# Kernel tuning notes

Measured on AMD Instinct MI355X. Metric: run time of the kernel, lower is better.

The kernel has to match this reference:

```python
import jax, jax.numpy as jnp
import numpy as np

B, S, H = 2, 2048, 1024
NH = 16
HD = H // NH  # 64
EPS = 1e-6
NEG = -1e9


def setup_inputs() -> dict:
    key = jax.random.key(0)
    ks = jax.random.split(key, 6)
    scale = 1.0 / np.sqrt(H)
    return {
        "enc": jax.random.normal(ks[0], (B, S, H), dtype=jnp.float32),
        "mask": jnp.ones((B, 1, S, S), dtype=jnp.float32),
        "W_Q": jax.random.normal(ks[1], (H, H), dtype=jnp.float32) * scale,
        "W_K": jax.random.normal(ks[2], (H, H), dtype=jnp.float32) * scale,
        "W_V": jax.random.normal(ks[3], (H, H), dtype=jnp.float32) * scale,
        "W_O": jax.random.normal(ks[4], (H, H), dtype=jnp.float32) * scale,
        "ln_w": jnp.ones((H,), dtype=jnp.float32),
        "ln_b": jnp.zeros((H,), dtype=jnp.float32),
    }


def reference(enc, mask, W_Q, W_K, W_V, W_O, ln_w, ln_b):
    residual = enc
    # projections (nn.Linear: x @ W.T), split heads -> [B, NH, S, HD]
    def proj(W):
        return (enc @ W.T).reshape(B, S, NH, HD).transpose(0, 2, 1, 3)
    Q, K, V = proj(W_Q), proj(W_K), proj(W_V)
    # scaled dot-product attention with mask
    attn_score = jnp.einsum("bhqd,bhkd->bhqk", Q, K) / jnp.sqrt(jnp.float32(HD))
    attn_score = jnp.where(mask == 0, jnp.float32(NEG), attn_score)
    attn_dist = jax.nn.softmax(attn_score, axis=-1)  # dropout_prob=0 -> identity
    out = jnp.einsum("bhqk,bhkd->bhqd", attn_dist, V)
    out = out.transpose(0, 2, 1, 3).reshape(B, S, H)
    # output projection + residual + LayerNorm(eps=1e-6)
    x = out @ W_O.T + residual
    mu = jnp.mean(x, axis=-1, keepdims=True)
    var = jnp.var(x, axis=-1, keepdims=True)
    y = (x - mu) / jnp.sqrt(var + EPS) * ln_w + ln_b
    return (y, attn_dist)
```

## Files before the change

### kernel.cpp

```cpp
#include <hip/hip_runtime.h>
#include <hip/hip_bf16.h>
#include <cstdint>

#define B_   2
#define S_   2048
#define H_   1024
#define NH_  16
#define HD_  64
#define YSIZE (B_*S_*H_)
#define ATTN_PER_BH ((size_t)S_*S_)

typedef __bf16 bf16x8 __attribute__((ext_vector_type(8)));
typedef __bf16 bf16x4_t __attribute__((ext_vector_type(4)));
typedef float f32x4 __attribute__((ext_vector_type(4)));

#define MFMA(a, b, c) __builtin_amdgcn_mfma_f32_16x16x32_bf16((a), (b), (c), 0, 0, 0)

__device__ __forceinline__ void gl2lds16(const void* g, void* lds) {
    __builtin_amdgcn_global_load_lds(
        (__attribute__((address_space(1))) void*)g,
        (__attribute__((address_space(3))) void*)lds,
        16, 0, 0);
}

__global__ __launch_bounds__(256) void k_convert(
    const float* __restrict__ enc, const float* __restrict__ wq,
    const float* __restrict__ wk, const float* __restrict__ wv,
    const float* __restrict__ wo,
    __bf16* __restrict__ encb, __bf16* __restrict__ wqb,
    __bf16* __restrict__ wkb, __bf16* __restrict__ wvb,
    __bf16* __restrict__ wob)
{
    size_t i = ((size_t)blockIdx.x * 256 + threadIdx.x) * 4;
    const float* src; __bf16* dst; size_t off;
    if (i < (size_t)YSIZE) { src = enc; dst = encb; off = i; }
    else {
        size_t j = i - YSIZE; int w = (int)(j >> 20); off = j & 1048575u;
        if      (w == 0) { src = wq; dst = wqb; }
        else if (w == 1) { src = wk; dst = wkb; }
        else if (w == 2) { src = wv; dst = wvb; }
        else             { src = wo; dst = wob; }
    }
    float4 v = *(const float4*)(src + off);
    bf16x4_t o;
    o[0] = (__bf16)v.x; o[1] = (__bf16)v.y; o[2] = (__bf16)v.z; o[3] = (__bf16)v.w;
    *(bf16x4_t*)(dst + off) = o;
}

template<int OUTF32>
__global__ __launch_bounds__(256) void k_gemm_nt(
    const __bf16* __restrict__ A, const __bf16* __restrict__ Bm,
    void* __restrict__ Cout, const float* __restrict__ resid,
    int K, int Nrs,
    unsigned Md, unsigned s1, unsigned s2, unsigned Nd, unsigned s3, unsigned s4)
{
    __shared__ __bf16 As[128 * 32];
    __shared__ __bf16 Bs[128 * 32];
    const int tid = threadIdx.x, l = tid & 63, w = tid >> 6;
    const int quad = l >> 4, l16 = l & 15;
    const int row0 = blockIdx.y * 128, col0 = blockIdx.x * 128;
    const int mbase = (w >> 1) * 64, nbase = (w & 1) * 64;

    f32x4 acc[4][4] = {};

    for (int k0 = 0; k0 < K; k0 += 32) {
#pragma unroll
        for (int i = 0; i < 2; ++i) {
            int lc = (w * 2 + i) * 64 + l;
            int r = lc >> 2, p = lc & 3;
            int c = p ^ ((r >> 1) & 3);
            gl2lds16(A + ((size_t)(row0 + r) * K + k0 + c * 8), As + (w * 2 + i) * 512);
            gl2lds16(Bm + ((size_t)(col0 + r) * K + k0 + c * 8), Bs + (w * 2 + i) * 512);
        }
        __syncthreads();
        bf16x8 af[4], bf[4];
#pragma unroll
        for (int mi = 0; mi < 4; ++mi) {
            int r = mbase + mi * 16 + l16;
            int c = quad ^ ((r >> 1) & 3);
            af[mi] = *(const bf16x8*)(As + r * 32 + c * 8);
        }
#pragma unroll
        for (int ni = 0; ni < 4; ++ni) {
            int r = nbase + ni * 16 + l16;
            int c = quad ^ ((r >> 1) & 3);
            bf[ni] = *(const bf16x8*)(Bs + r * 32 + c * 8);
        }
#pragma unroll
        for (int mi = 0; mi < 4; ++mi)
#pragma unroll
            for (int ni = 0; ni < 4; ++ni)
                acc[mi][ni] = MFMA(af[mi], bf[ni], acc[mi][ni]);
        __syncthreads();
    }

#pragma unroll
    for (int mi = 0; mi < 4; ++mi)
#pragma unroll
        for (int ni = 0; ni < 4; ++ni)
#pragma unroll
            for (int rr = 0; rr < 4; ++rr) {
                unsigned gm = row0 + mbase + mi * 16 + quad * 4 + rr;
                unsigned gn = col0 + nbase + ni * 16 + l16;
                size_t addr = (size_t)(gm / Md) * s1 + (size_t)(gm % Md) * s2
                            + (size_t)(gn / Nd) * s3 + (size_t)(gn % Nd) * s4;
                float v = acc[mi][ni][rr];
                if (OUTF32) {
                    ((float*)Cout)[addr] = v + resid[(size_t)gm * Nrs + gn];
                } else {
                    ((__bf16*)Cout)[addr] = (__bf16)v;
                }
            }
}

__global__ __launch_bounds__(256) void k_attn(
    const __bf16* __restrict__ Qb, const __bf16* __restrict__ Kb,
    const __bf16* __restrict__ Vtb, const float* __restrict__ mask,
    float* __restrict__ attn, __bf16* __restrict__ AO)
{
    __shared__ __bf16 Qs[128 * 64];
    __shared__ __bf16 Ks[128 * 64];
    __shared__ __bf16 Vts[64 * 128];
    __shared__ __bf16 Ps[128 * 64];

    const int tid = threadIdx.x, l = tid & 63, w = tid >> 6;
    const int quad = l >> 4, l16 = l & 15;
    const int q0 = blockIdx.x * 128, h = blockIdx.y, b = blockIdx.z;
    const size_t headQK = (size_t)(b * NH_ + h) * S_ * HD_;
    const __bf16* Qh = Qb + headQK;
    const __bf16* Kh = Kb + headQK;
    const __bf16* Vth = Vtb + (size_t)h * HD_ * (B_ * S_) + (size_t)b * S_;
    const float* maskb = mask + (size_t)b * ATTN_PER_BH;
    float* attnb = attn + (size_t)(b * NH_ + h) * ATTN_PER_BH;

#pragma unroll
    for (int i = 0; i < 4; ++i) {
        int lc = (w * 4 + i) * 64 + l;
        int r = lc >> 3, p = lc & 7, c = p ^ (r & 7);
        gl2lds16(Qh + ((size_t)(q0 + r) * HD_ + c * 8), Qs + (w * 4 + i) * 512);
    }

    float rs[2][4] = {{0.f, 0.f, 0.f, 0.f}, {0.f, 0.f, 0.f, 0.f}};

    for (int kt = 0; kt < 16; ++kt) {
#pragma unroll
        for (int i = 0; i < 4; ++i) {
            int lc = (w * 4 + i) * 64 + l;
            int r = lc >> 3, p = lc & 7, c = p ^ (r & 7);
            gl2lds16(Kh + ((size_t)(kt * 128 + r) * HD_ + c * 8), Ks + (w * 4 + i) * 512);
        }
        __syncthreads();

        f32x4 sa[2][8] = {};
#pragma unroll
        for (int ks = 0; ks < 2; ++ks) {
            bf16x8 af[2];
#pragma unroll
            for (int mi = 0; mi < 2; ++mi) {
                int r = w * 32 + mi * 16 + l16;
                int c = (ks * 4 + quad) ^ (r & 7);
                af[mi] = *(const bf16x8*)(Qs + r * 64 + c * 8);
            }
#pragma unroll
            for (int nt = 0; nt < 8; ++nt) {
                int r = nt * 16 + l16;
                int c = (ks * 4 + quad) ^ (r & 7);
                bf16x8 bv = *(const bf16x8*)(Ks + r * 64 + c * 8);
#pragma unroll
                for (int mi = 0; mi < 2; ++mi)
                    sa[mi][nt] = MFMA(af[mi], bv, sa[mi][nt]);
            }
        }
#pragma unroll
        for (int mi = 0; mi < 2; ++mi) {
            int rowg = q0 + w * 32 + mi * 16 + quad * 4;
#pragma unroll
            for (int nt = 0; nt < 8; ++nt) {
                int col = kt * 128 + nt * 16 + l16;
#pragma unroll
                for (int rr = 0; rr < 4; ++rr) {
                    float mv = maskb[(size_t)(rowg + rr) * S_ + col];
                    float p = (mv == 0.f) ? 0.f : __expf(sa[mi][nt][rr] * 0.125f);
                    rs[mi][rr] += p;
                }
            }
        }
        __syncthreads();
    }

    float inv_l[2][4];
#pragma unroll
    for (int mi = 0; mi < 2; ++mi)
#pragma unroll
        for (int rr = 0; rr < 4; ++rr) {
            float v = rs[mi][rr];
            v += __shfl_xor(v, 1); v += __shfl_xor(v, 2);
            v += __shfl_xor(v, 4); v += __shfl_xor(v, 8);
            inv_l[mi][rr] = 1.0f / v;
        }

    f32x4 oa[2][4] = {};

    for (int kt = 0; kt < 16; ++kt) {
#pragma unroll
        for (int i = 0; i < 4; ++i) {
            int lc = (w * 4 + i) * 64 + l;
            int r = lc >> 3, p = lc & 7, c = p ^ (r & 7);
            gl2lds16(Kh + ((size_t)(kt * 128 + r) * HD_ + c * 8), Ks + (w * 4 + i) * 512);
        }
#pragma unroll
        for (int i = 0; i < 4; ++i) {
            int lc = (w * 4 + i) * 64 + l;
            int r = lc >> 4, p = lc & 15, c = p ^ (r & 15);
            gl2lds16(Vth + ((size_t)r * (B_ * S_) + kt * 128 + c * 8), Vts + (w * 4 + i) * 512);
        }
        __syncthreads();

        f32x4 sa[2][8] = {};
#pragma unroll
        for (int ks = 0; ks < 2; ++ks) {
            bf16x8 af[2];
#pragma unroll
            for (int mi = 0; mi < 2; ++mi) {
                int r = w * 32 + mi * 16 + l16;
                int c = (ks * 4 + quad) ^ (r & 7);
                af[mi] = *(const bf16x8*)(Qs + r * 64 + c * 8);
            }
#pragma unroll
            for (int nt = 0; nt < 8; ++nt) {
                int r = nt * 16 + l16;
                int c = (ks * 4 + quad) ^ (r & 7);
                bf16x8 bv = *(const bf16x8*)(Ks + r * 64 + c * 8);
#pragma unroll
                for (int mi = 0; mi < 2; ++mi)
                    sa[mi][nt] = MFMA(af[mi], bv, sa[mi][nt]);
            }
        }
#pragma unroll
        for (int mi = 0; mi < 2; ++mi) {
            int rowg = q0 + w * 32 + mi * 16 + quad * 4;
#pragma unroll
            for (int nt = 0; nt < 8; ++nt) {
                int col = kt * 128 + nt * 16 + l16;
#pragma unroll
                for (int rr = 0; rr < 4; ++rr) {
                    float mv = maskb[(size_t)(rowg + rr) * S_ + col];
                    float p = (mv == 0.f) ? 0.f
                            : __expf(sa[mi][nt][rr] * 0.125f) * inv_l[mi][rr];
                    sa[mi][nt][rr] = p;
                    attnb[(size_t)(rowg + rr) * S_ + col] = p;
                }
            }
        }
#pragma unroll
        for (int mi = 0; mi < 2; ++mi) {
            int m0 = w * 32 + mi * 16 + quad * 4;
#pragma unroll
            for (int nt = 0; nt < 4; ++nt) {
                int kl = nt * 16 + l16;
#pragma unroll
                for (int rr = 0; rr < 4; ++rr) {
                    int m = m0 + rr;
                    int ch = (kl >> 3) ^ (m & 7);
                    Ps[m * 64 + ch * 8 + (kl & 7)] = (__bf16)sa[mi][nt][rr];
                }
            }
        }
        __syncthreads();
#pragma unroll
        for (int ks = 0; ks < 2; ++ks) {
            bf16x8 af[2];
#pragma unroll
            for (int mi = 0; mi < 2; ++mi) {
                int r = w * 32 + mi * 16 + l16;
                int c = (ks * 4 + quad) ^ (r & 7);
                af[mi] = *(const bf16x8*)(Ps + r * 64 + c * 8);
            }
#pragma unroll
            for (int nt = 0; nt < 4; ++nt) {
                int dr = nt * 16 + l16;
                int vc = (ks * 4 + quad) ^ (dr & 15);
                bf16x8 bv = *(const bf16x8*)(Vts + dr * 128 + vc * 8);
#pragma unroll
                for (int mi = 0; mi < 2; ++mi)
                    oa[mi][nt] = MFMA(af[mi], bv, oa[mi][nt]);
            }
        }
        __syncthreads();
#pragma unroll
        for (int mi = 0; mi < 2; ++mi) {
            int m0 = w * 32 + mi * 16 + quad * 4;
#pragma unroll
            for (int nt = 4; nt < 8; ++nt) {
                int kl = (nt - 4) * 16 + l16;
#pragma unroll
                for (int rr = 0; rr < 4; ++rr) {
                    int m = m0 + rr;
                    int ch = (kl >> 3) ^ (m & 7);
                    Ps[m * 64 + ch * 8 + (kl & 7)] = (__bf16)sa[mi][nt][rr];
                }
            }
        }
        __syncthreads();
#pragma unroll
        for (int ks = 0; ks < 2; ++ks) {
            bf16x8 af[2];
#pragma unroll
            for (int mi = 0; mi < 2; ++mi) {
                int r = w * 32 + mi * 16 + l16;
                int c = (ks * 4 + quad) ^ (r & 7);
                af[mi] = *(const bf16x8*)(Ps + r * 64 + c * 8);
            }
#pragma unroll
            for (int nt = 0; nt < 4; ++nt) {
                int dr = nt * 16 + l16;
                int vc = (8 + ks * 4 + quad) ^ (dr & 15);
                bf16x8 bv = *(const bf16x8*)(Vts + dr * 128 + vc * 8);
#pragma unroll
                for (int mi = 0; mi < 2; ++mi)
                    oa[mi][nt] = MFMA(af[mi], bv, oa[mi][nt]);
            }
        }
        __syncthreads();
    }

#pragma unroll
    for (int mi = 0; mi < 2; ++mi)
#pragma unroll
        for (int nt = 0; nt < 4; ++nt)
#pragma unroll
            for (int rr = 0; rr < 4; ++rr) {
                int sg = b * S_ + q0 + w * 32 + mi * 16 + quad * 4 + rr;
                int f = h * HD_ + nt * 16 + l16;
                AO[(size_t)sg * H_ + f] = (__bf16)oa[mi][nt][rr];
            }
}

__global__ __launch_bounds__(256) void k_ln(
    float* __restrict__ x, const float* __restrict__ lw, const float* __restrict__ lb)
{
    __shared__ float red[8];
    const int row = blockIdx.x, tid = threadIdx.x;
    float4 v = *(float4*)(x + (size_t)row * H_ + tid * 4);
    float s = v.x + v.y + v.z + v.w;
    float ss = v.x * v.x + v.y * v.y + v.z * v.z + v.w * v.w;
#pragma unroll
    for (int o = 1; o < 64; o <<= 1) { s += __shfl_xor(s, o); ss += __shfl_xor(ss, o); }
    const int w = tid >> 6;
    if ((tid & 63) == 0) { red[w] = s; red[4 + w] = ss; }
    __syncthreads();
    s = red[0] + red[1] + red[2] + red[3];
    ss = red[4] + red[5] + red[6] + red[7];
    float mu = s * (1.0f / H_);
    float var = ss * (1.0f / H_) - mu * mu;
    float rstd = rsqrtf(var + 1e-6f);
    float4 wv = *(const float4*)(lw + tid * 4);
    float4 bv = *(const float4*)(lb + tid * 4);
    float4 y;
    y.x = (v.x - mu) * rstd * wv.x + bv.x;
    y.y = (v.y - mu) * rstd * wv.y + bv.y;
    y.z = (v.z - mu) * rstd * wv.z + bv.z;
    y.w = (v.w - mu) * rstd * wv.w + bv.w;
    *(float4*)(x + (size_t)row * H_ + tid * 4) = y;
}

extern "C" void kernel_launch(void* const* d_in, const int* in_sizes, int n_in,
                              void* d_out, int out_size, void* d_ws, size_t ws_size,
                              hipStream_t stream)
{
    const float* enc  = (const float*)d_in[0];
    const float* mask = (const float*)d_in[1];
    const float* WQ   = (const float*)d_in[2];
    const float* WK   = (const float*)d_in[3];
    const float* WV   = (const float*)d_in[4];
    const float* WO   = (const float*)d_in[5];
    const float* lnw  = (const float*)d_in[6];
    const float* lnb  = (const float*)d_in[7];

    float* y    = (float*)d_out;
    float* attn = y + YSIZE;

    char* ws = (char*)d_ws;
    __bf16* encb = (__bf16*)(ws);
    __bf16* wqb  = (__bf16*)(ws + (8ull  << 20));
    __bf16* wkb  = (__bf16*)(ws + (10ull << 20));
    __bf16* wvb  = (__bf16*)(ws + (12ull << 20));
    __bf16* wob  = (__bf16*)(ws + (14ull << 20));
    __bf16* Qb   = (__bf16*)(ws + (16ull << 20));
    __bf16* Kb   = (__bf16*)(ws + (24ull << 20));
    __bf16* Vtb  = (__bf16*)(ws + (32ull << 20));
    __bf16* AO   = (__bf16*)(ws + (40ull << 20));

    k_convert<<<8192, 256, 0, stream>>>(enc, WQ, WK, WV, WO, encb, wqb, wkb, wvb, wob);

    dim3 gQK(8, 32);
    k_gemm_nt<0><<<gQK, 256, 0, stream>>>(encb, wqb, Qb, nullptr, H_, 0,
                                          2048u, 2097152u, 64u, 64u, 131072u, 1u);
    k_gemm_nt<0><<<gQK, 256, 0, stream>>>(encb, wkb, Kb, nullptr, H_, 0,
                                          2048u, 2097152u, 64u, 64u, 131072u, 1u);
    dim3 gV(32, 8);
    k_gemm_nt<0><<<gV, 256, 0, stream>>>(wvb, encb, Vtb, nullptr, H_, 0,
                                         4096u, 0u, 4096u, 4096u, 0u, 1u);

    dim3 gA(S_ / 128, NH_, B_);
    k_attn<<<gA, 256, 0, stream>>>(Qb, Kb, Vtb, mask, attn, AO);

    k_gemm_nt<1><<<gQK, 256, 0, stream>>>(AO, wob, y, enc, H_, H_,
                                          4096u, 0u, 1024u, 1024u, 0u, 1u);

    k_ln<<<YSIZE / H_, 256, 0, stream>>>(y, lnw, lnb);
}
```

Before: 1.172 ms.

## Bit-pack attention mask and prefetch K/V tiles through registers

Adds a pre-pass that packs the fp32 mask into a bitmask, so the attention kernel reads 1 bit per element instead of 4 bytes in both passes, with a fast path when the whole tile is unmasked. K and V tiles for the next step are prefetched into registers and written to LDS after compute, replacing direct global-to-LDS loads. Some barriers between the P-staging and PV phases are removed because each warp only touches its own rows, and launch bounds request 2 blocks per CU. This adds an extra kernel launch and reuses the workspace region of the converted input for the bits.

```diff
diff --git a/kernel.cpp b/kernel.cpp
--- a/kernel.cpp
+++ b/kernel.cpp
@@ -47,6 +47,29 @@
     *(bf16x4_t*)(dst + off) = o;
 }
 
+__global__ __launch_bounds__(256) void k_maskbits(
+    const float* __restrict__ mask, unsigned long long* __restrict__ mbits)
+{
+    __shared__ unsigned char byt[256];
+    const int row = blockIdx.x, t = threadIdx.x;
+    const float* mrow = mask + (size_t)row * S_;
+    float4 a = *(const float4*)(mrow + t * 8);
+    float4 b = *(const float4*)(mrow + t * 8 + 4);
+    unsigned v = (a.x != 0.f ? 1u : 0u)  | (a.y != 0.f ? 2u : 0u)
+               | (a.z != 0.f ? 4u : 0u)  | (a.w != 0.f ? 8u : 0u)
+               | (b.x != 0.f ? 16u : 0u) | (b.y != 0.f ? 32u : 0u)
+               | (b.z != 0.f ? 64u : 0u) | (b.w != 0.f ? 128u : 0u);
+    byt[t] = (unsigned char)v;
+    __syncthreads();
+    if (t < 32) {
+        unsigned long long w = 0;
+#pragma unroll
+        for (int j = 0; j < 8; ++j)
+            w |= (unsigned long long)byt[t * 8 + j] << (8 * j);
+        mbits[(size_t)row * 32 + t] = w;
+    }
+}
+
 template<int OUTF32>
 __global__ __launch_bounds__(256) void k_gemm_nt(
     const __bf16* __restrict__ A, const __bf16* __restrict__ Bm,
@@ -113,9 +136,9 @@
             }
 }
 
-__global__ __launch_bounds__(256) void k_attn(
+__global__ __launch_bounds__(256, 2) void k_attn(
     const __bf16* __restrict__ Qb, const __bf16* __restrict__ Kb,
-    const __bf16* __restrict__ Vtb, const float* __restrict__ mask,
+    const __bf16* __restrict__ Vtb, const unsigned long long* __restrict__ mbits,
     float* __restrict__ attn, __bf16* __restrict__ AO)
 {
     __shared__ __bf16 Qs[128 * 64];
@@ -130,7 +153,7 @@
     const __bf16* Qh = Qb + headQK;
     const __bf16* Kh = Kb + headQK;
     const __bf16* Vth = Vtb + (size_t)h * HD_ * (B_ * S_) + (size_t)b * S_;
-    const float* maskb = mask + (size_t)b * ATTN_PER_BH;
+    const unsigned long long* mrow = mbits + (size_t)b * S_ * 32;
     float* attnb = attn + (size_t)(b * NH_ + h) * ATTN_PER_BH;
 
 #pragma unroll
@@ -140,16 +163,47 @@
         gl2lds16(Qh + ((size_t)(q0 + r) * HD_ + c * 8), Qs + (w * 4 + i) * 512);
     }
 
+    bf16x8 kreg[4], vreg[4];
+    auto loadK = [&](int kt) {
+#pragma unroll
+        for (int j = 0; j < 4; ++j) {
+            int lc = j * 256 + tid;
+            kreg[j] = *(const bf16x8*)(Kh + (size_t)kt * (128 * HD_) + lc * 8);
+        }
+    };
+    auto writeK = [&]() {
+#pragma unroll
+        for (int j = 0; j < 4; ++j) {
+            int lc = j * 256 + tid;
+            int r = lc >> 3, p = lc & 7, c = p ^ (r & 7);
+            *(bf16x8*)(Ks + r * 64 + c * 8) = kreg[j];
+        }
+    };
+    auto loadV = [&](int kt) {
+#pragma unroll
+        for (int j = 0; j < 4; ++j) {
+            int lc = j * 256 + tid;
+            int r = lc >> 4, p = lc & 15;
+            vreg[j] = *(const bf16x8*)(Vth + (size_t)r * (B_ * S_) + kt * 128 + p * 8);
+        }
+    };
+    auto writeV = [&]() {
+#pragma unroll
+        for (int j = 0; j < 4; ++j) {
+            int lc = j * 256 + tid;
+            int r = lc >> 4, p = lc & 15, c = p ^ (r & 15);
+            *(bf16x8*)(Vts + r * 128 + c * 8) = vreg[j];
+        }
+    };
+
     float rs[2][4] = {{0.f, 0.f, 0.f, 0.f}, {0.f, 0.f, 0.f, 0.f}};
 
+    loadK(0);
+    writeK();
+    __syncthreads();
+
     for (int kt = 0; kt < 16; ++kt) {
-#pragma unroll
-        for (int i = 0; i < 4; ++i) {
-            int lc = (w * 4 + i) * 64 + l;
-            int r = lc >> 3, p = lc & 7, c = p ^ (r & 7);
-            gl2lds16(Kh + ((size_t)(kt * 128 + r) * HD_ + c * 8), Ks + (w * 4 + i) * 512);
-        }
-        __syncthreads();
+        if (kt < 15) loadK(kt + 1);
 
         f32x4 sa[2][8] = {};
 #pragma unroll
@@ -171,20 +225,43 @@
                     sa[mi][nt] = MFMA(af[mi], bv, sa[mi][nt]);
             }
         }
-#pragma unroll
-        for (int mi = 0; mi < 2; ++mi) {
-            int rowg = q0 + w * 32 + mi * 16 + quad * 4;
-#pragma unroll
-            for (int nt = 0; nt < 8; ++nt) {
-                int col = kt * 128 + nt * 16 + l16;
+
+        unsigned long long mwx[2][4], mwy[2][4];
+        unsigned long long andv = ~0ull;
+#pragma unroll
+        for (int mi = 0; mi < 2; ++mi)
+#pragma unroll
+            for (int rr = 0; rr < 4; ++rr) {
+                int rowq = q0 + w * 32 + mi * 16 + quad * 4 + rr;
+                ulonglong2 mv = *(const ulonglong2*)(mrow + (size_t)rowq * 32 + kt * 2);
+                mwx[mi][rr] = mv.x; mwy[mi][rr] = mv.y;
+                andv &= mv.x & mv.y;
+            }
+        if (__all(andv == ~0ull)) {
+#pragma unroll
+            for (int mi = 0; mi < 2; ++mi)
+#pragma unroll
+                for (int nt = 0; nt < 8; ++nt)
+#pragma unroll
+                    for (int rr = 0; rr < 4; ++rr)
+                        rs[mi][rr] += __expf(sa[mi][nt][rr] * 0.125f);
+        } else {
+#pragma unroll
+            for (int mi = 0; mi < 2; ++mi)
 #pragma unroll
                 for (int rr = 0; rr < 4; ++rr) {
-                    float mv = maskb[(size_t)(rowg + rr) * S_ + col];
-                    float p = (mv == 0.f) ? 0.f : __expf(sa[mi][nt][rr] * 0.125f);
-                    rs[mi][rr] += p;
+                    unsigned long long tx = mwx[mi][rr] >> l16;
+                    unsigned long long ty = mwy[mi][rr] >> l16;
+#pragma unroll
+                    for (int nt = 0; nt < 8; ++nt) {
+                        unsigned long long t = (nt & 4) ? ty : tx;
+                        unsigned ok = (unsigned)(t >> ((nt & 3) * 16)) & 1u;
+                        rs[mi][rr] += ok ? __expf(sa[mi][nt][rr] * 0.125f) : 0.f;
+                    }
                 }
-            }
-        }
+        }
+        __syncthreads();
+        if (kt < 15) writeK();
         __syncthreads();
     }
 
@@ -201,20 +278,12 @@
 
     f32x4 oa[2][4] = {};
 
+    loadK(0); loadV(0);
+    writeK(); writeV();
+    __syncthreads();
+
     for (int kt = 0; kt < 16; ++kt) {
-#pragma unroll
-        for (int i = 0; i < 4; ++i) {
-            int lc = (w * 4 + i) * 64 + l;
-            int r = lc >> 3, p = lc & 7, c = p ^ (r & 7);
-            gl2lds16(Kh + ((size_t)(kt * 128 + r) * HD_ + c * 8), Ks + (w * 4 + i) * 512);
-        }
-#pragma unroll
-        for (int i = 0; i < 4; ++i) {
-            int lc = (w * 4 + i) * 64 + l;
-            int r = lc >> 4, p = lc & 15, c = p ^ (r & 15);
-            gl2lds16(Vth + ((size_t)r * (B_ * S_) + kt * 128 + c * 8), Vts + (w * 4 + i) * 512);
-        }
-        __syncthreads();
+        if (kt < 15) { loadK(kt + 1); loadV(kt + 1); }
 
         f32x4 sa[2][8] = {};
 #pragma unroll
@@ -236,22 +305,52 @@
                     sa[mi][nt] = MFMA(af[mi], bv, sa[mi][nt]);
             }
         }
-#pragma unroll
-        for (int mi = 0; mi < 2; ++mi) {
-            int rowg = q0 + w * 32 + mi * 16 + quad * 4;
-#pragma unroll
-            for (int nt = 0; nt < 8; ++nt) {
-                int col = kt * 128 + nt * 16 + l16;
+
+        unsigned long long mwx[2][4], mwy[2][4];
+        unsigned long long andv = ~0ull;
+#pragma unroll
+        for (int mi = 0; mi < 2; ++mi)
+#pragma unroll
+            for (int rr = 0; rr < 4; ++rr) {
+                int rowq = q0 + w * 32 + mi * 16 + quad * 4 + rr;
+                ulonglong2 mv = *(const ulonglong2*)(mrow + (size_t)rowq * 32 + kt * 2);
+                mwx[mi][rr] = mv.x; mwy[mi][rr] = mv.y;
+                andv &= mv.x & mv.y;
+            }
+        if (__all(andv == ~0ull)) {
+#pragma unroll
+            for (int mi = 0; mi < 2; ++mi)
 #pragma unroll
                 for (int rr = 0; rr < 4; ++rr) {
-                    float mv = maskb[(size_t)(rowg + rr) * S_ + col];
-                    float p = (mv == 0.f) ? 0.f
-                            : __expf(sa[mi][nt][rr] * 0.125f) * inv_l[mi][rr];
-                    sa[mi][nt][rr] = p;
-                    attnb[(size_t)(rowg + rr) * S_ + col] = p;
+                    int rowg = q0 + w * 32 + mi * 16 + quad * 4 + rr;
+                    float il = inv_l[mi][rr];
+#pragma unroll
+                    for (int nt = 0; nt < 8; ++nt) {
+                        float p = __expf(sa[mi][nt][rr] * 0.125f) * il;
+                        sa[mi][nt][rr] = p;
+                        attnb[(size_t)rowg * S_ + kt * 128 + nt * 16 + l16] = p;
+                    }
                 }
-            }
-        }
+        } else {
+#pragma unroll
+            for (int mi = 0; mi < 2; ++mi)
+#pragma unroll
+                for (int rr = 0; rr < 4; ++rr) {
+                    int rowg = q0 + w * 32 + mi * 16 + quad * 4 + rr;
+                    float il = inv_l[mi][rr];
+                    unsigned long long tx = mwx[mi][rr] >> l16;
+                    unsigned long long ty = mwy[mi][rr] >> l16;
+#pragma unroll
+                    for (int nt = 0; nt < 8; ++nt) {
+                        unsigned long long t = (nt & 4) ? ty : tx;
+                        unsigned ok = (unsigned)(t >> ((nt & 3) * 16)) & 1u;
+                        float p = ok ? __expf(sa[mi][nt][rr] * 0.125f) * il : 0.f;
+                        sa[mi][nt][rr] = p;
+                        attnb[(size_t)rowg * S_ + kt * 128 + nt * 16 + l16] = p;
+                    }
+                }
+        }
+
 #pragma unroll
         for (int mi = 0; mi < 2; ++mi) {
             int m0 = w * 32 + mi * 16 + quad * 4;
@@ -266,7 +365,6 @@
                 }
             }
         }
-        __syncthreads();
 #pragma unroll
         for (int ks = 0; ks < 2; ++ks) {
             bf16x8 af[2];
@@ -286,7 +384,6 @@
                     oa[mi][nt] = MFMA(af[mi], bv, oa[mi][nt]);
             }
         }
-        __syncthreads();
 #pragma unroll
         for (int mi = 0; mi < 2; ++mi) {
             int m0 = w * 32 + mi * 16 + quad * 4;
@@ -301,7 +398,6 @@
                 }
             }
         }
-        __syncthreads();
 #pragma unroll
         for (int ks = 0; ks < 2; ++ks) {
             bf16x8 af[2];
@@ -321,6 +417,8 @@
                     oa[mi][nt] = MFMA(af[mi], bv, oa[mi][nt]);
             }
         }
+        __syncthreads();
+        if (kt < 15) { writeK(); writeV(); }
         __syncthreads();
     }
 
@@ -390,6 +488,7 @@
     __bf16* Kb   = (__bf16*)(ws + (24ull << 20));
     __bf16* Vtb  = (__bf16*)(ws + (32ull << 20));
     __bf16* AO   = (__bf16*)(ws + (40ull << 20));
+    unsigned long long* mbits = (unsigned long long*)ws;
 
     k_convert<<<8192, 256, 0, stream>>>(enc, WQ, WK, WV, WO, encb, wqb, wkb, wvb, wob);
 
@@ -402,8 +501,10 @@
     k_gemm_nt<0><<<gV, 256, 0, stream>>>(wvb, encb, Vtb, nullptr, H_, 0,
                                          4096u, 0u, 4096u, 4096u, 0u, 1u);
 
+    k_maskbits<<<B_ * S_, 256, 0, stream>>>(mask, mbits);
+
     dim3 gA(S_ / 128, NH_, B_);
-    k_attn<<<gA, 256, 0, stream>>>(Qb, Kb, Vtb, mask, attn, AO);
+    k_attn<<<gA, 256, 0, stream>>>(Qb, Kb, Vtb, mbits, attn, AO);
 
     k_gemm_nt<1><<<gQK, 256, 0, stream>>>(AO, wob, y, enc, H_, H_,
                                           4096u, 0u, 1024u, 1024u, 0u, 1u);
```

Result: faster. 1.074 ms (-8.4%).
